# Performance work log

Hardware: AMD Instinct MI355X
Metric: run time of the kernel (lower is better)

## Reference

```python
import jax, jax.numpy as jnp
import numpy as np

NU, NI, ED, H = 30000, 10000, 64, 4
D = ED * H            # fusion_dim = 256
N = NU + NI           # total graph nodes
E = 100000            # edges
B = 8192              # scored (user, wine) pairs
NST, SD = 4, 64       # side tokens / side token dim
NEG = -1e30


def setup_inputs():
    key = jax.random.key(0)
    ks = iter(jax.random.split(key, 64))

    def w(*shape):
        return jax.random.normal(next(ks), shape, jnp.float32) * 0.05

    return {
        "user": jax.random.randint(next(ks), (B,), 0, NU),
        "wine": jax.random.randint(next(ks), (B,), 0, NI),
        "edge_index": jax.random.randint(next(ks), (2, E), 0, N),
        "keep_edge": jax.random.uniform(next(ks), (E,)) > 0.2,   # edge_dropout keep mask
        "node_mask": jax.random.uniform(next(ks), (N,)) < 0.2,   # mask-autoencoding mask
        "user_emb": w(NU, ED),
        "wine_emb": w(NI, ED),
        "up_w": w(ED, D), "up_b": w(D),
        "wp_w": w(ED, D), "wp_b": w(D),
        "sf_proj_w": w(SD, D), "sf_proj_b": w(D),
        "sf_q_w": w(D, D), "sf_q_b": w(D),
        "sf_k_w": w(D, D), "sf_k_b": w(D),
        "sf_v_w": w(D, D), "sf_v_b": w(D),
        "sf_o_w": w(D, D), "sf_o_b": w(D),
        "sf_fc_w": w(2 * D, D), "sf_fc_b": w(D),
        "g_w": w(D, D), "g_b": w(D),
        "t_q_w": w(D, H * D), "t_q_b": w(H * D),
        "t_k_w": w(D, H * D), "t_k_b": w(H * D),
        "t_v_w": w(D, H * D), "t_v_b": w(H * D),
        "t_skip_w": w(D, D), "t_skip_b": w(D),
        "fc_w": w(2 * D, 1), "fc_b": w(1),
        "ae_w": w(D, D), "ae_b": w(D),
        "ep_w": w(2 * D, 1), "ep_b": w(1),
        "wine_side_features": jax.random.normal(next(ks), (NI, NST, SD), jnp.float32),
    }


def _forward(user, wine, edge_index, keep_edge, node_mask,
             user_emb, wine_emb, up_w, up_b, wp_w, wp_b,
             sf_proj_w, sf_proj_b, sf_q_w, sf_q_b, sf_k_w, sf_k_b,
             sf_v_w, sf_v_b, sf_o_w, sf_o_b, sf_fc_w, sf_fc_b,
             g_w, g_b, t_q_w, t_q_b, t_k_w, t_k_b, t_v_w, t_v_b,
             t_skip_w, t_skip_b, fc_w, fc_b, ae_w, ae_b, ep_w, ep_b,
             wine_side_features):
    u_proj = user_emb @ up_w + up_b                       # [NU, D]
    w_proj = wine_emb @ wp_w + wp_b                       # [NI, D]

    # WineSideFusion: single-head attention of wine embedding over side tokens
    side = wine_side_features @ sf_proj_w + sf_proj_b     # [NI, T, D]
    q = w_proj @ sf_q_w + sf_q_b                          # [NI, D]
    k = side @ sf_k_w + sf_k_b                            # [NI, T, D]
    v = side @ sf_v_w + sf_v_b
    attn = jax.nn.softmax(jnp.einsum('nd,ntd->nt', q, k) / jnp.sqrt(jnp.float32(D)), axis=-1)
    ao = jnp.einsum('nt,ntd->nd', attn, v) @ sf_o_w + sf_o_b
    fused = jnp.concatenate([w_proj, ao], axis=1) @ sf_fc_w + sf_fc_b

    x = jnp.concatenate([u_proj, fused], axis=0)          # [N, D]
    src, dst = edge_index[0], edge_index[1]
    ew = keep_edge.astype(x.dtype)                        # edge dropout as 0/1 weights

    # GCNConv (add self loops, symmetric norm)
    deg = jax.ops.segment_sum(ew, dst, num_segments=N) + 1.0
    dinv = jax.lax.rsqrt(deg)
    norm = dinv[src] * dinv[dst] * ew                     # [E]
    xw = x @ g_w                                          # [N, D]
    agg = jax.ops.segment_sum(xw[src] * norm[:, None], dst, num_segments=N)
    x = agg + xw * (dinv * dinv)[:, None] + g_b

    # TransformerConv(heads=H, concat=False): mean over heads + skip
    qh = (x @ t_q_w + t_q_b).reshape(N, H, D)
    kh = (x @ t_k_w + t_k_b).reshape(N, H, D)
    vh = (x @ t_v_w + t_v_b).reshape(N, H, D)
    logits = jnp.einsum('ehd,ehd->eh', qh[dst], kh[src]) / jnp.sqrt(jnp.float32(D))
    logits = jnp.where(keep_edge[:, None], logits, NEG)
    m = jax.ops.segment_max(logits, dst, num_segments=N)  # [N, H]
    m = jnp.where(m < NEG / 2, 0.0, m)                    # guard empty segments
    e = jnp.exp(logits - m[dst]) * ew[:, None]            # [E, H]
    den = jax.ops.segment_sum(e, dst, num_segments=N)     # [N, H]
    num = jax.ops.segment_sum(e[:, :, None] * vh[src], dst, num_segments=N)  # [N, H, D]
    attn_out = num / jnp.maximum(den, 1e-16)[:, :, None]
    x = attn_out.mean(axis=1) + x @ t_skip_w + t_skip_b   # [N, D]

    # Masked autoencoding: masked rows are zeroed, then autoencoded -> recon = bias
    maskf = node_mask.astype(x.dtype)
    recon = ae_b                                          # 0 @ ae_w + ae_b
    diff = recon[None, :] - x                             # [N, D]
    recon_loss = jnp.sum(maskf[:, None] * diff * diff) / (jnp.sum(maskf) * D)

    u_out = x[user]                                       # [B, D]
    w_out = x[wine + NU]                                  # [B, D]
    pair = jnp.concatenate([u_out, w_out], axis=1)        # [B, 2D]

    edge_score = jax.nn.sigmoid(pair @ ep_w + ep_b)       # [B, 1]
    edge_pred_loss = jnp.mean((edge_score - 1.0) ** 2)

    score = jax.nn.sigmoid((pair @ fc_w + fc_b).squeeze(-1)) * 4.0 + 1.0  # [B]
    return score, recon_loss, edge_pred_loss


def reference(user, wine, edge_index, keep_edge, node_mask,
              user_emb, wine_emb, up_w, up_b, wp_w, wp_b,
              sf_proj_w, sf_proj_b, sf_q_w, sf_q_b, sf_k_w, sf_k_b,
              sf_v_w, sf_v_b, sf_o_w, sf_o_b, sf_fc_w, sf_fc_b,
              g_w, g_b, t_q_w, t_q_b, t_k_w, t_k_b, t_v_w, t_v_b,
              t_skip_w, t_skip_b, fc_w, fc_b, ae_w, ae_b, ep_w, ep_b,
              wine_side_features):
    return _forward(user, wine, edge_index, keep_edge, node_mask,
                    user_emb, wine_emb, up_w, up_b, wp_w, wp_b,
                    sf_proj_w, sf_proj_b, sf_q_w, sf_q_b, sf_k_w, sf_k_b,
                    sf_v_w, sf_v_b, sf_o_w, sf_o_b, sf_fc_w, sf_fc_b,
                    g_w, g_b, t_q_w, t_q_b, t_k_w, t_k_b, t_v_w, t_v_b,
                    t_skip_w, t_skip_b, fc_w, fc_b, ae_w, ae_b, ep_w, ep_b,
                    wine_side_features)
```

## Files before the change

### kernel.cpp

```cpp
#include <hip/hip_runtime.h>
#include <stdint.h>

typedef unsigned short u16;
typedef unsigned char u8;
typedef __attribute__((ext_vector_type(8))) short bf16x8;
typedef __attribute__((ext_vector_type(4))) float f32x4;

#define NU_C 30000
#define NI_C 10000
#define N_C  40000
#define E_C  100000
#define B_C  8192

static __device__ __forceinline__ float bf2f(u16 u) {
    union { unsigned int i; float f; } c; c.i = ((unsigned int)u) << 16; return c.f;
}
static __device__ __forceinline__ u16 f2bf(float f) {
    union { float f; unsigned int i; } c; c.f = f;
    return (u16)((c.i + 0x7FFFu + ((c.i >> 16) & 1u)) >> 16);
}
static __device__ __forceinline__ float wave_sum(float v) {
#pragma unroll
    for (int off = 32; off > 0; off >>= 1) v += __shfl_xor(v, off);
    return v;
}
static __device__ __forceinline__ float group_sum16(float v) {
#pragma unroll
    for (int off = 8; off > 0; off >>= 1) v += __shfl_xor(v, off);
    return v;
}
static __device__ __forceinline__ float dot16(const bf16x8 a0, const bf16x8 a1,
                                              const bf16x8 b0, const bf16x8 b1) {
    float p = 0.f;
#pragma unroll
    for (int j = 0; j < 8; ++j) p = fmaf(bf2f((u16)a0[j]), bf2f((u16)b0[j]), p);
#pragma unroll
    for (int j = 0; j < 8; ++j) p = fmaf(bf2f((u16)a1[j]), bf2f((u16)b1[j]), p);
    return p;
}

__global__ void zero_kernel(unsigned int* p, int n) {
    int i = blockIdx.x * 256 + threadIdx.x;
    if (i < n) p[i] = 0u;
}
__global__ void fillval_kernel(float* p, int n, float v) {
    int i = blockIdx.x * 256 + threadIdx.x;
    if (i < n) p[i] = v;
}

__global__ void detect_kernel(const unsigned int* a, int n, int* flag) {
    int i = blockIdx.x * 256 + threadIdx.x;
    if (i >= n) return;
    unsigned int v = a[i];
    int f = 0;
    if (v > 1u) f |= 1;
    if (v != 0u && v != 0x3F800000u) f |= 2;
    if (f) atomicOr(flag, f);
}
__global__ void conv_masks_kernel(const void* keep_raw, const void* nm_raw,
                                  u8* km, u8* nm, int E, int N, const int* flag)
{
    int i = blockIdx.x * 256 + threadIdx.x;
    const int f = *flag;
    if (i < E) {
        u8 r;
        if ((f & 1) == 0)      r = ((const int*)keep_raw)[i] != 0;
        else if ((f & 2) == 0) r = ((const float*)keep_raw)[i] != 0.f;
        else                   r = ((const u8*)keep_raw)[i] != 0;
        km[i] = r;
    }
    int j = i - E;
    if (j >= 0 && j < N) {
        u8 r;
        if ((f & 1) == 0)      r = ((const int*)nm_raw)[j] != 0;
        else if ((f & 2) == 0) r = ((const float*)nm_raw)[j] != 0.f;
        else                   r = ((const u8*)nm_raw)[j] != 0;
        nm[j] = r;
    }
}

__global__ void conv3_kernel(const float* __restrict__ a, int na4,
                             const float* __restrict__ b, int nb4,
                             const float* __restrict__ c, int nc4,
                             u16* __restrict__ oa, u16* __restrict__ ob, u16* __restrict__ oc)
{
    int tot = na4 + nb4 + nc4;
    for (int i = blockIdx.x * 256 + threadIdx.x; i < tot; i += gridDim.x * 256) {
        const float* s; u16* o; int j = i;
        if (j < na4) { s = a; o = oa; }
        else if ((j -= na4) < nb4) { s = b; o = ob; }
        else { j -= nb4; s = c; o = oc; }
        float4 v = *(const float4*)&s[(size_t)j * 4];
        ushort4 r;
        r.x = f2bf(v.x); r.y = f2bf(v.y); r.z = f2bf(v.z); r.w = f2bf(v.w);
        *(ushort4*)&o[(size_t)j * 4] = r;
    }
}

#define WT_ELEMS 1359872
__device__ const int wd_prefix[23] = {0,16384,32768,49152,114688,180224,245760,311296,442368,
    507904,573440,638976,704512,770048,835584,901120,966656,1032192,1097728,1163264,1228800,
    1294336,1359872};
__device__ const u8  wd_src[22]  = {0,1,2,3,4,5,6,7,8,9,10,11,12,10,11,12,10,11,12,10,11,12};
__device__ const short wd_ldw[22]= {256,256,256,256,256,256,256,256,256,256,
    1024,1024,1024,1024,1024,1024,1024,1024,1024,1024,1024,1024};
__device__ const short wd_coff[22]={0,0,0,0,0,0,0,0,0,0, 0,0,0, 256,256,256, 512,512,512, 768,768,768};
__device__ const short wd_kmask[22]={63,63,63,255,255,255,255,511,255,255,
    255,255,255,255,255,255,255,255,255,255,255,255};
__device__ const u8  wd_ksh[22] = {6,6,6,8,8,8,8,9,8,8, 8,8,8,8,8,8,8,8,8,8,8,8};

__global__ __launch_bounds__(256)
void wtrans_kernel(const float* w0, const float* w1, const float* w2, const float* w3,
                   const float* w4, const float* w5, const float* w6, const float* w7,
                   const float* w8, const float* w9, const float* w10, const float* w11,
                   const float* w12, u16* __restrict__ WT)
{
    int idx = blockIdx.x * 256 + threadIdx.x;
    if (idx >= WT_ELEMS) return;
    int d = 0;
    while (wd_prefix[d + 1] <= idx) ++d;
    const int local = idx - wd_prefix[d];
    const int k = local & wd_kmask[d];
    const int n = local >> wd_ksh[d];
    const float* s;
    switch (wd_src[d]) {
        case 0: s = w0; break; case 1: s = w1; break; case 2: s = w2; break;
        case 3: s = w3; break; case 4: s = w4; break; case 5: s = w5; break;
        case 6: s = w6; break; case 7: s = w7; break; case 8: s = w8; break;
        case 9: s = w9; break; case 10: s = w10; break; case 11: s = w11; break;
        default: s = w12; break;
    }
    WT[idx] = f2bf(s[(size_t)k * wd_ldw[d] + wd_coff[d] + n]);
}

__global__ void prep_bias_kernel(const float* sfk_b, const float* sfv_b,
                                 const float* tq_b, const float* tk_b, const float* tv_b,
                                 float* kvb, float* qkvb)
{
    int i = blockIdx.x * 256 + threadIdx.x;
    if (i < 512) kvb[i] = i < 256 ? sfk_b[i] : sfv_b[i - 256];
    if (i < 3072) {
        int h = i / 768, j = i - h * 768;
        qkvb[i] = j < 256 ? tq_b[h * 256 + j]
                : (j < 512 ? tk_b[h * 256 + j - 256] : tv_b[h * 256 + j - 512]);
    }
}

template <typename OT>
__global__ __launch_bounds__(512)
void mgemm_kernel(const u16* __restrict__ A, int lda,
                  const u16* __restrict__ WT,
                  const float* __restrict__ bias,
                  OT* __restrict__ C, int ldc,
                  int M, int N, int K)
{
    __shared__ __align__(16) u16 As[256][72];
    __shared__ __align__(16) u16 Bs[128][72];
    const int t = threadIdx.x;
    const int wid = t >> 6, lane = t & 63;
    const int wr = wid >> 1, wc = wid & 1;
    const int lr = lane & 15, lg = lane >> 4;
    const int gx = gridDim.x;
    const int nwg = gx * gridDim.y;
    const int orig = blockIdx.y * gx + blockIdx.x;
    const int q8 = nwg >> 3, r8 = nwg & 7;
    const int xcd = orig & 7, oidx = orig >> 3;
    const int swzb = (xcd < r8 ? xcd * (q8 + 1) : r8 * (q8 + 1) + (xcd - r8) * q8) + oidx;
    const int row0 = (swzb / gx) * 256, col0 = (swzb % gx) * 128;
    const int sra = t >> 1, sha = (t & 1) * 32;
    const int srb = t >> 2, shb = (t & 3) * 16;
    const bool avalid = (row0 + sra) < M;
    const u16* aptr = &A[(size_t)min(row0 + sra, M - 1) * lda];
    const u16* bptr = &WT[(size_t)(col0 + srb) * K];
    const bf16x8 z = {0, 0, 0, 0, 0, 0, 0, 0};
    f32x4 acc[4][4] = {};
    bf16x8 ra[4], rb[2];

    auto gload = [&](int k0) {
#pragma unroll
        for (int j = 0; j < 4; ++j)
            ra[j] = avalid ? *(const bf16x8*)&aptr[k0 + sha + j * 8] : z;
#pragma unroll
        for (int j = 0; j < 2; ++j)
            rb[j] = *(const bf16x8*)&bptr[k0 + shb + j * 8];
    };
    auto swrite = [&]() {
#pragma unroll
        for (int j = 0; j < 4; ++j)
            *(bf16x8*)&As[sra][sha + j * 8] = ra[j];
#pragma unroll
        for (int j = 0; j < 2; ++j)
            *(bf16x8*)&Bs[srb][shb + j * 8] = rb[j];
    };
    auto compute = [&]() {
#pragma unroll
        for (int kk = 0; kk < 2; ++kk) {
            bf16x8 af[4], bfr[4];
#pragma unroll
            for (int m = 0; m < 4; ++m)
                af[m] = *(const bf16x8*)&As[wr * 64 + m * 16 + lr][kk * 32 + lg * 8];
#pragma unroll
            for (int n = 0; n < 4; ++n)
                bfr[n] = *(const bf16x8*)&Bs[wc * 64 + n * 16 + lr][kk * 32 + lg * 8];
#pragma unroll
            for (int m = 0; m < 4; ++m)
#pragma unroll
                for (int n = 0; n < 4; ++n)
                    acc[m][n] = __builtin_amdgcn_mfma_f32_16x16x32_bf16(af[m], bfr[n], acc[m][n], 0, 0, 0);
        }
    };

    gload(0);
    swrite();
    __syncthreads();
    for (int k0 = 64; k0 < K; k0 += 64) {
        gload(k0);
        compute();
        __syncthreads();
        swrite();
        __syncthreads();
    }
    compute();

#pragma unroll
    for (int m = 0; m < 4; ++m) {
#pragma unroll
        for (int r = 0; r < 4; ++r) {
            int row = row0 + wr * 64 + m * 16 + lg * 4 + r;
            if (row >= M) continue;
#pragma unroll
            for (int n = 0; n < 4; ++n) {
                int col = col0 + wc * 64 + n * 16 + lr;
                float v = acc[m][n][r];
                if (bias) v += bias[col];
                if constexpr (sizeof(OT) == 4) C[(size_t)row * ldc + col] = v;
                else C[(size_t)row * ldc + col] = f2bf(v);
            }
        }
    }
}

__global__ __launch_bounds__(256)
void side_attn_kernel(const u16* __restrict__ q, const u16* __restrict__ kv,
                      u16* __restrict__ ao, int NI)
{
    const int wid = threadIdx.x >> 6, lane = threadIdx.x & 63;
    const int n = blockIdx.x * 4 + wid;
    if (n >= NI) return;
    const ushort4 qu = *(const ushort4*)&q[(size_t)n * 256 + lane * 4];
    const float q0 = bf2f(qu.x), q1 = bf2f(qu.y), q2 = bf2f(qu.z), q3 = bf2f(qu.w);
    float logit[4];
#pragma unroll
    for (int tk = 0; tk < 4; ++tk) {
        const ushort4 ku = *(const ushort4*)&kv[((size_t)n * 4 + tk) * 512 + lane * 4];
        float p = q0 * bf2f(ku.x) + q1 * bf2f(ku.y) + q2 * bf2f(ku.z) + q3 * bf2f(ku.w);
        logit[tk] = wave_sum(p) * (1.f / 16.f);
    }
    float mx = fmaxf(fmaxf(logit[0], logit[1]), fmaxf(logit[2], logit[3]));
    float e[4], den = 0.f;
#pragma unroll
    for (int tk = 0; tk < 4; ++tk) { e[tk] = __expf(logit[tk] - mx); den += e[tk]; }
    const float inv = 1.f / den;
    float o0 = 0.f, o1 = 0.f, o2 = 0.f, o3 = 0.f;
#pragma unroll
    for (int tk = 0; tk < 4; ++tk) {
        const ushort4 vu = *(const ushort4*)&kv[((size_t)n * 4 + tk) * 512 + 256 + lane * 4];
        const float w = e[tk] * inv;
        o0 = fmaf(w, bf2f(vu.x), o0); o1 = fmaf(w, bf2f(vu.y), o1);
        o2 = fmaf(w, bf2f(vu.z), o2); o3 = fmaf(w, bf2f(vu.w), o3);
    }
    ushort4 o;
    o.x = f2bf(o0); o.y = f2bf(o1); o.z = f2bf(o2); o.w = f2bf(o3);
    *(ushort4*)&ao[(size_t)n * 256 + lane * 4] = o;
}

__global__ void count_kernel(const int* __restrict__ dst, const u8* __restrict__ keep,
                             int* __restrict__ cnt, float* __restrict__ degw, int E)
{
    int e = blockIdx.x * 256 + threadIdx.x;
    if (e >= E) return;
    int d = dst[e];
    atomicAdd(&cnt[d], 1);
    if (keep[e]) atomicAdd(&degw[d], 1.f);
}

__global__ void dinv_kernel(const float* __restrict__ degw, float* __restrict__ dinv, int N)
{
    int n = blockIdx.x * 256 + threadIdx.x;
    if (n < N) dinv[n] = rsqrtf(degw[n] + 1.f);
}

__global__ __launch_bounds__(1024)
void scan_kernel(const int* __restrict__ cnt, int* __restrict__ rs, int n)
{
    __shared__ int wsum[17];
    __shared__ int s_run;
    const int t = threadIdx.x, lane = t & 63, wid = t >> 6;
    if (t == 0) s_run = 0;
    __syncthreads();
    for (int base = 0; base < n; base += 1024) {
        int i = base + t;
        int v = (i < n) ? cnt[i] : 0;
        int x = v;
#pragma unroll
        for (int off = 1; off < 64; off <<= 1) {
            int y = __shfl_up(x, off);
            if (lane >= off) x += y;
        }
        if (lane == 63) wsum[wid] = x;
        __syncthreads();
        if (t == 0) {
            int a = 0;
            for (int j = 0; j < 16; ++j) { int tmp = wsum[j]; wsum[j] = a; a += tmp; }
            wsum[16] = a;
        }
        __syncthreads();
        if (i < n) rs[i] = s_run + wsum[wid] + x - v;
        __syncthreads();
        if (t == 0) s_run += wsum[16];
        __syncthreads();
    }
    if (t == 0) rs[n] = s_run;
}

__global__ void fill_kernel(const int* __restrict__ dst, const int* __restrict__ rs,
                            int* __restrict__ cursor, int* __restrict__ eid, int E)
{
    int e = blockIdx.x * 256 + threadIdx.x;
    if (e >= E) return;
    int d = dst[e];
    int p = atomicAdd(&cursor[d], 1);
    eid[rs[d] + p] = e;
}

__global__ void sort_kernel(const int* __restrict__ rs, int* __restrict__ eid, int N)
{
    int n = blockIdx.x * 256 + threadIdx.x;
    if (n >= N) return;
    const int b = rs[n], len = rs[n + 1] - b;
    for (int i = 1; i < len; ++i) {
        int key = eid[b + i];
        int j = i - 1;
        while (j >= 0 && eid[b + j] > key) { eid[b + j + 1] = eid[b + j]; --j; }
        eid[b + j + 1] = key;
    }
}

__global__ void edge_prep_kernel(const int* __restrict__ eid, const int* __restrict__ src,
                                 const int* __restrict__ dst, const u8* __restrict__ keep,
                                 const float* __restrict__ dinv,
                                 int* __restrict__ ssrc, float* __restrict__ wnorm, int E)
{
    int i = blockIdx.x * 256 + threadIdx.x;
    if (i >= E) return;
    const int e = eid[i];
    const int s = src[e];
    const u8 k = keep[e];
    ssrc[i] = s * 2 + (int)k;
    wnorm[i] = k ? dinv[s] * dinv[dst[e]] : 0.f;
}

__global__ __launch_bounds__(256)
void gcn_kernel(const u16* __restrict__ xw, const int* __restrict__ ssrc,
                const float* __restrict__ wnorm, const int* __restrict__ rs,
                const float* __restrict__ dinv, const float* __restrict__ gb,
                u16* __restrict__ xout, int N)
{
    const int wid = threadIdx.x >> 6, lane = threadIdx.x & 63;
    const int n = blockIdx.x * 4 + wid;
    if (n >= N) return;
    const float di = dinv[n];
    const float dii = di * di;
    const ushort4 own = *(const ushort4*)&xw[(size_t)n * 256 + lane * 4];
    float a0 = bf2f(own.x) * dii, a1 = bf2f(own.y) * dii;
    float a2 = bf2f(own.z) * dii, a3 = bf2f(own.w) * dii;
    const int e0 = rs[n], e1 = rs[n + 1];
    int i = e0;
    for (; i + 1 < e1; i += 2) {
        const float wa = wnorm[i], wb = wnorm[i + 1];
        const int sa = ssrc[i] >> 1, sb = ssrc[i + 1] >> 1;
        const ushort4 ra = *(const ushort4*)&xw[(size_t)sa * 256 + lane * 4];
        const ushort4 rb = *(const ushort4*)&xw[(size_t)sb * 256 + lane * 4];
        a0 = fmaf(bf2f(rb.x), wb, fmaf(bf2f(ra.x), wa, a0));
        a1 = fmaf(bf2f(rb.y), wb, fmaf(bf2f(ra.y), wa, a1));
        a2 = fmaf(bf2f(rb.z), wb, fmaf(bf2f(ra.z), wa, a2));
        a3 = fmaf(bf2f(rb.w), wb, fmaf(bf2f(ra.w), wa, a3));
    }
    if (i < e1) {
        const float wa = wnorm[i];
        const int sa = ssrc[i] >> 1;
        const ushort4 r = *(const ushort4*)&xw[(size_t)sa * 256 + lane * 4];
        a0 = fmaf(bf2f(r.x), wa, a0); a1 = fmaf(bf2f(r.y), wa, a1);
        a2 = fmaf(bf2f(r.z), wa, a2); a3 = fmaf(bf2f(r.w), wa, a3);
    }
    const float4 g = *(const float4*)&gb[lane * 4];
    ushort4 o;
    o.x = f2bf(a0 + g.x); o.y = f2bf(a1 + g.y);
    o.z = f2bf(a2 + g.z); o.w = f2bf(a3 + g.w);
    *(ushort4*)&xout[(size_t)n * 256 + lane * 4] = o;
}

__global__ __launch_bounds__(256)
void tconv_head_kernel(const u16* __restrict__ qkv, const int* __restrict__ ssrc,
                       const int* __restrict__ rs, float* __restrict__ xacc, int N)
{
    const int wid = threadIdx.x >> 6, lane = threadIdx.x & 63;
    const int g = lane >> 4, s = lane & 15;
    const int n = blockIdx.x * 16 + wid * 4 + g;
    if (n >= N) return;
    const bf16x8 qa = *(const bf16x8*)&qkv[(size_t)n * 768 + s * 16];
    const bf16x8 qb = *(const bf16x8*)&qkv[(size_t)n * 768 + s * 16 + 8];
    const int e0 = rs[n], e1 = rs[n + 1];
    float m = -1e30f, den = 0.f;
    float ac[16] = {};
    int i = e0;
    for (; i + 1 < e1; i += 2) {
        const int va = ssrc[i], vb = ssrc[i + 1];
        const size_t sa = (size_t)(va >> 1) * 768, sb = (size_t)(vb >> 1) * 768;
        const float ewa = (float)(va & 1), ewb = (float)(vb & 1);
        const bf16x8 ka0 = *(const bf16x8*)&qkv[sa + 256 + s * 16];
        const bf16x8 ka1 = *(const bf16x8*)&qkv[sa + 256 + s * 16 + 8];
        const bf16x8 kb0 = *(const bf16x8*)&qkv[sb + 256 + s * 16];
        const bf16x8 kb1 = *(const bf16x8*)&qkv[sb + 256 + s * 16 + 8];
        const bf16x8 xa0 = *(const bf16x8*)&qkv[sa + 512 + s * 16];
        const bf16x8 xa1 = *(const bf16x8*)&qkv[sa + 512 + s * 16 + 8];
        const bf16x8 xb0 = *(const bf16x8*)&qkv[sb + 512 + s * 16];
        const bf16x8 xb1 = *(const bf16x8*)&qkv[sb + 512 + s * 16 + 8];
        float pa = group_sum16(dot16(qa, qb, ka0, ka1)) * (1.f / 16.f);
        float pb = group_sum16(dot16(qa, qb, kb0, kb1)) * (1.f / 16.f);
        {
            const float mn = fmaxf(m, pa);
            const float sc = __expf(m - mn);
            const float w = __expf(pa - mn) * ewa;
            den = den * sc + w;
#pragma unroll
            for (int j = 0; j < 8; ++j) ac[j] = fmaf(w, bf2f((u16)xa0[j]), ac[j] * sc);
#pragma unroll
            for (int j = 0; j < 8; ++j) ac[8 + j] = fmaf(w, bf2f((u16)xa1[j]), ac[8 + j] * sc);
            m = mn;
        }
        {
            const float mn = fmaxf(m, pb);
            const float sc = __expf(m - mn);
            const float w = __expf(pb - mn) * ewb;
            den = den * sc + w;
#pragma unroll
            for (int j = 0; j < 8; ++j) ac[j] = fmaf(w, bf2f((u16)xb0[j]), ac[j] * sc);
#pragma unroll
            for (int j = 0; j < 8; ++j) ac[8 + j] = fmaf(w, bf2f((u16)xb1[j]), ac[8 + j] * sc);
            m = mn;
        }
    }
    if (i < e1) {
        const int va = ssrc[i];
        const size_t sa = (size_t)(va >> 1) * 768;
        const float ewa = (float)(va & 1);
        const bf16x8 ka0 = *(const bf16x8*)&qkv[sa + 256 + s * 16];
        const bf16x8 ka1 = *(const bf16x8*)&qkv[sa + 256 + s * 16 + 8];
        const bf16x8 xa0 = *(const bf16x8*)&qkv[sa + 512 + s * 16];
        const bf16x8 xa1 = *(const bf16x8*)&qkv[sa + 512 + s * 16 + 8];
        float pa = group_sum16(dot16(qa, qb, ka0, ka1)) * (1.f / 16.f);
        const float mn = fmaxf(m, pa);
        const float sc = __expf(m - mn);
        const float w = __expf(pa - mn) * ewa;
        den = den * sc + w;
#pragma unroll
        for (int j = 0; j < 8; ++j) ac[j] = fmaf(w, bf2f((u16)xa0[j]), ac[j] * sc);
#pragma unroll
        for (int j = 0; j < 8; ++j) ac[8 + j] = fmaf(w, bf2f((u16)xa1[j]), ac[8 + j] * sc);
    }
    const float inv = 0.25f / fmaxf(den, 1e-16f);
    float4* p4 = (float4*)&xacc[(size_t)n * 256 + s * 16];
#pragma unroll
    for (int q = 0; q < 4; ++q) {
        float4 cur = p4[q];
        cur.x += ac[q * 4 + 0] * inv; cur.y += ac[q * 4 + 1] * inv;
        cur.z += ac[q * 4 + 2] * inv; cur.w += ac[q * 4 + 3] * inv;
        p4[q] = cur;
    }
}

__global__ __launch_bounds__(256)
void recon_kernel(const float* __restrict__ x, const u8* __restrict__ mask,
                  const float* __restrict__ aeb,
                  float* __restrict__ rblkS, float* __restrict__ rblkC, int N)
{
    const int total = N * 256;
    float s = 0.f, c = 0.f;
    for (int idx = blockIdx.x * 256 + threadIdx.x; idx < total; idx += gridDim.x * 256) {
        const int n = idx >> 8, d = idx & 255;
        if (mask[n]) {
            const float diff = aeb[d] - x[idx];
            s = fmaf(diff, diff, s);
            if (d == 0) c += 1.f;
        }
    }
    s = wave_sum(s); c = wave_sum(c);
    __shared__ float ss[4], cc[4];
    const int lane = threadIdx.x & 63, wid = threadIdx.x >> 6;
    if (lane == 0) { ss[wid] = s; cc[wid] = c; }
    __syncthreads();
    if (threadIdx.x == 0) {
        rblkS[blockIdx.x] = ss[0] + ss[1] + ss[2] + ss[3];
        rblkC[blockIdx.x] = cc[0] + cc[1] + cc[2] + cc[3];
    }
}

__global__ __launch_bounds__(256)
void score_kernel(const float* __restrict__ x, const int* __restrict__ user,
                  const int* __restrict__ wine,
                  const float* __restrict__ epw, const float* __restrict__ epb,
                  const float* __restrict__ fcw, const float* __restrict__ fcb,
                  float* __restrict__ out, float* __restrict__ sblk, int B)
{
    __shared__ float sep[4];
    const int wid = threadIdx.x >> 6, lane = threadIdx.x & 63;
    const int b = blockIdx.x * 4 + wid;
    if (b < B) {
        const size_t u = (size_t)user[b];
        const size_t w = (size_t)wine[b] + NU_C;
        const float4 xu = *(const float4*)&x[u * 256 + lane * 4];
        const float4 xw = *(const float4*)&x[w * 256 + lane * 4];
        const float4 e1 = *(const float4*)&epw[lane * 4];
        const float4 e2 = *(const float4*)&epw[256 + lane * 4];
        const float4 f1 = *(const float4*)&fcw[lane * 4];
        const float4 f2 = *(const float4*)&fcw[256 + lane * 4];
        float pep = xu.x * e1.x + xu.y * e1.y + xu.z * e1.z + xu.w * e1.w
                  + xw.x * e2.x + xw.y * e2.y + xw.z * e2.z + xw.w * e2.w;
        float pfc = xu.x * f1.x + xu.y * f1.y + xu.z * f1.z + xu.w * f1.w
                  + xw.x * f2.x + xw.y * f2.y + xw.z * f2.z + xw.w * f2.w;
        pep = wave_sum(pep); pfc = wave_sum(pfc);
        if (lane == 0) {
            const float es = 1.f / (1.f + __expf(-(pep + epb[0])));
            sep[wid] = (es - 1.f) * (es - 1.f);
            out[b] = 1.f / (1.f + __expf(-(pfc + fcb[0]))) * 4.f + 1.f;
        }
    } else if (lane == 0) {
        sep[wid] = 0.f;
    }
    __syncthreads();
    if (threadIdx.x == 0) sblk[blockIdx.x] = sep[0] + sep[1] + sep[2] + sep[3];
}

__global__ __launch_bounds__(1024)
void final_reduce_kernel(const float* __restrict__ rblkS, const float* __restrict__ rblkC,
                         const float* __restrict__ sblk, float* __restrict__ out, int B)
{
    const int t = threadIdx.x, lane = t & 63, wid = t >> 6;
    float s = rblkS[t] + rblkS[t + 1024];
    float c = rblkC[t] + rblkC[t + 1024];
    float p = sblk[t] + sblk[t + 1024];
    s = wave_sum(s); c = wave_sum(c); p = wave_sum(p);
    __shared__ float ss[16], cc[16], pp[16];
    if (lane == 0) { ss[wid] = s; cc[wid] = c; pp[wid] = p; }
    __syncthreads();
    if (t == 0) {
        float S = 0.f, C = 0.f, P = 0.f;
        for (int i = 0; i < 16; ++i) { S += ss[i]; C += cc[i]; P += pp[i]; }
        out[B] = S / (C * 256.f);
        out[B + 1] = P / (float)B;
    }
}

extern "C" void kernel_launch(void* const* d_in, const int* in_sizes, int n_in,
                              void* d_out, int out_size, void* d_ws, size_t ws_size,
                              hipStream_t stream)
{
    const int* user = (const int*)d_in[0];
    const int* wine = (const int*)d_in[1];
    const int* e_src = (const int*)d_in[2];
    const int* e_dst = e_src + E_C;
    const void* keep_raw  = d_in[3];
    const void* nmask_raw = d_in[4];
    const float* user_emb = (const float*)d_in[5];
    const float* wine_emb = (const float*)d_in[6];
    const float* up_w = (const float*)d_in[7];
    const float* up_b = (const float*)d_in[8];
    const float* wp_w = (const float*)d_in[9];
    const float* wp_b = (const float*)d_in[10];
    const float* sf_proj_w = (const float*)d_in[11];
    const float* sf_proj_b = (const float*)d_in[12];
    const float* sf_q_w = (const float*)d_in[13];
    const float* sf_q_b = (const float*)d_in[14];
    const float* sf_k_w = (const float*)d_in[15];
    const float* sf_k_b = (const float*)d_in[16];
    const float* sf_v_w = (const float*)d_in[17];
    const float* sf_v_b = (const float*)d_in[18];
    const float* sf_o_w = (const float*)d_in[19];
    const float* sf_o_b = (const float*)d_in[20];
    const float* sf_fc_w = (const float*)d_in[21];
    const float* sf_fc_b = (const float*)d_in[22];
    const float* g_w = (const float*)d_in[23];
    const float* g_b = (const float*)d_in[24];
    const float* t_q_w = (const float*)d_in[25];
    const float* t_q_b = (const float*)d_in[26];
    const float* t_k_w = (const float*)d_in[27];
    const float* t_k_b = (const float*)d_in[28];
    const float* t_v_w = (const float*)d_in[29];
    const float* t_v_b = (const float*)d_in[30];
    const float* t_skip_w = (const float*)d_in[31];
    const float* t_skip_b = (const float*)d_in[32];
    const float* fc_w = (const float*)d_in[33];
    const float* fc_b = (const float*)d_in[34];
    const float* ae_b = (const float*)d_in[36];
    const float* ep_w = (const float*)d_in[37];
    const float* ep_b = (const float*)d_in[38];
    const float* wsf = (const float*)d_in[39];
    float* out = (float*)d_out;
    char* ws = (char*)d_ws;

    size_t off = 0;
    auto take = [&](size_t b) { size_t r = off; off += (b + 255) & ~(size_t)255; return r; };
    const size_t o_xb     = take((size_t)N_C * 256 * 2);
    const size_t o_cnt    = take((size_t)N_C * 4);
    const size_t o_degw   = take((size_t)N_C * 4);
    const size_t o_cursor = take((size_t)N_C * 4);
    const size_t o_scal   = take(256);
    const size_t o_rowst  = take((size_t)(N_C + 1) * 4);
    const size_t o_dinv   = take((size_t)N_C * 4);
    const size_t o_eid    = take((size_t)E_C * 4);
    const size_t o_ssrc   = take((size_t)E_C * 4);
    const size_t o_wnorm  = take((size_t)E_C * 4);
    const size_t o_kmask  = take((size_t)E_C);
    const size_t o_nmask  = take((size_t)N_C);
    const size_t o_rblkS  = take(2048 * 4);
    const size_t o_rblkC  = take(2048 * 4);
    const size_t o_sblk   = take(2048 * 4);
    const size_t o_wt     = take((size_t)WT_ELEMS * 2);
    const size_t o_bias   = take(3584 * 4);
    const size_t ARENA    = 102400000;
    const size_t o_arena  = take(ARENA);
    const size_t NEED = off;

    if (ws_size < NEED) {
        fillval_kernel<<<dim3((out_size + 255) / 256), 256, 0, stream>>>(
            out, out_size, (float)((double)ws_size / (1024.0 * 1024.0)));
        return;
    }

    u16*   xb     = (u16*)  (ws + o_xb);
    int*   cnt    = (int*)  (ws + o_cnt);
    float* degw   = (float*)(ws + o_degw);
    int*   cursor = (int*)  (ws + o_cursor);
    int*   flag   = (int*)  (ws + o_scal);
    int*   rowst  = (int*)  (ws + o_rowst);
    float* dinvb  = (float*)(ws + o_dinv);
    int*   eid    = (int*)  (ws + o_eid);
    int*   ssrc   = (int*)  (ws + o_ssrc);
    float* wnorm  = (float*)(ws + o_wnorm);
    u8*    kmask  = (u8*)   (ws + o_kmask);
    u8*    nmaskb = (u8*)   (ws + o_nmask);
    float* rblkS  = (float*)(ws + o_rblkS);
    float* rblkC  = (float*)(ws + o_rblkC);
    float* sblk   = (float*)(ws + o_sblk);
    u16*   WT     = (u16*)  (ws + o_wt);
    float* kvb    = (float*)(ws + o_bias);
    float* qkvb   = kvb + 512;

    u16* wt_up   = WT + 0;
    u16* wt_wp   = WT + 16384;
    u16* wt_proj = WT + 32768;
    u16* wt_sfq  = WT + 49152;
    u16* wt_sfkv = WT + 114688;
    u16* wt_sfo  = WT + 245760;
    u16* wt_sffc = WT + 311296;
    u16* wt_g    = WT + 442368;
    u16* wt_skip = WT + 507904;
    u16* wt_qkv  = WT + 573440;

    u16* ue16  = (u16*)(ws + o_arena);
    u16* we16  = (u16*)(ws + o_arena + 3840000);
    u16* wsf16 = (u16*)(ws + o_arena + 5120000);
    u16* cat   = (u16*)(ws + o_arena + 10240000);
    u16* side  = (u16*)(ws + o_arena + 20480000);
    u16* qbuf  = (u16*)(ws + o_arena + 40960000);
    u16* kvbuf = (u16*)(ws + o_arena + 46080000);
    u16* aobuf = (u16*)(ws + o_arena + 87040000);
    u16* xw    = (u16*)(ws + o_arena);
    u16* qkvh  = (u16*)(ws + o_arena);
    float* xacc = (float*)(ws + o_arena + 61440000);

    const int zero_words = (3 * N_C * 4 + 256) / 4;
    zero_kernel<<<dim3((zero_words + 255) / 256), 256, 0, stream>>>((unsigned int*)cnt, zero_words);

    detect_kernel<<<dim3((E_C / 4 + 255) / 256), 256, 0, stream>>>((const unsigned int*)keep_raw, E_C / 4, flag);
    conv_masks_kernel<<<dim3((E_C + N_C + 255) / 256), 256, 0, stream>>>(keep_raw, nmask_raw, kmask, nmaskb, E_C, N_C, flag);

    conv3_kernel<<<dim3(2048), 256, 0, stream>>>(user_emb, NU_C * 16, wine_emb, NI_C * 16,
                                                 wsf, N_C * 16, ue16, we16, wsf16);
    wtrans_kernel<<<dim3(WT_ELEMS / 256), 256, 0, stream>>>(up_w, wp_w, sf_proj_w, sf_q_w,
        sf_k_w, sf_v_w, sf_o_w, sf_fc_w, g_w, t_skip_w, t_q_w, t_k_w, t_v_w, WT);
    prep_bias_kernel<<<dim3(12), 256, 0, stream>>>(sf_k_b, sf_v_b, t_q_b, t_k_b, t_v_b, kvb, qkvb);

    mgemm_kernel<u16><<<dim3(2, 118), 512, 0, stream>>>(ue16, 64, wt_up, up_b, xb, 256, NU_C, 256, 64);
    mgemm_kernel<u16><<<dim3(2, 40), 512, 0, stream>>>(we16, 64, wt_wp, wp_b, cat, 512, NI_C, 256, 64);
    mgemm_kernel<u16><<<dim3(2, 157), 512, 0, stream>>>(wsf16, 64, wt_proj, sf_proj_b, side, 256, N_C, 256, 64);
    mgemm_kernel<u16><<<dim3(2, 40), 512, 0, stream>>>(cat, 512, wt_sfq, sf_q_b, qbuf, 256, NI_C, 256, 256);
    mgemm_kernel<u16><<<dim3(4, 157), 512, 0, stream>>>(side, 256, wt_sfkv, kvb, kvbuf, 512, N_C, 512, 256);
    side_attn_kernel<<<dim3(2500), 256, 0, stream>>>(qbuf, kvbuf, aobuf, NI_C);
    mgemm_kernel<u16><<<dim3(2, 40), 512, 0, stream>>>(aobuf, 256, wt_sfo, sf_o_b, cat + 256, 512, NI_C, 256, 256);
    mgemm_kernel<u16><<<dim3(2, 40), 512, 0, stream>>>(cat, 512, wt_sffc, sf_fc_b, xb + (size_t)NU_C * 256, 256, NI_C, 256, 512);

    count_kernel<<<dim3((E_C + 255) / 256), 256, 0, stream>>>(e_dst, kmask, cnt, degw, E_C);
    dinv_kernel<<<dim3((N_C + 255) / 256), 256, 0, stream>>>(degw, dinvb, N_C);
    scan_kernel<<<dim3(1), 1024, 0, stream>>>(cnt, rowst, N_C);
    fill_kernel<<<dim3((E_C + 255) / 256), 256, 0, stream>>>(e_dst, rowst, cursor, eid, E_C);
    sort_kernel<<<dim3((N_C + 255) / 256), 256, 0, stream>>>(rowst, eid, N_C);
    edge_prep_kernel<<<dim3((E_C + 255) / 256), 256, 0, stream>>>(eid, e_src, e_dst, kmask, dinvb, ssrc, wnorm, E_C);

    mgemm_kernel<u16><<<dim3(2, 157), 512, 0, stream>>>(xb, 256, wt_g, nullptr, xw, 256, N_C, 256, 256);
    gcn_kernel<<<dim3(N_C / 4), 256, 0, stream>>>(xw, ssrc, wnorm, rowst, dinvb, g_b, xb, N_C);

    mgemm_kernel<float><<<dim3(2, 157), 512, 0, stream>>>(xb, 256, wt_skip, t_skip_b, xacc, 256, N_C, 256, 256);
    for (int h = 0; h < 4; ++h) {
        mgemm_kernel<u16><<<dim3(6, 157), 512, 0, stream>>>(xb, 256, wt_qkv + h * 196608,
                                                            qkvb + h * 768, qkvh, 768, N_C, 768, 256);
        tconv_head_kernel<<<dim3(N_C / 16), 256, 0, stream>>>(qkvh, ssrc, rowst, xacc, N_C);
    }

    recon_kernel<<<dim3(2048), 256, 0, stream>>>(xacc, nmaskb, ae_b, rblkS, rblkC, N_C);
    score_kernel<<<dim3(2048), 256, 0, stream>>>(xacc, user, wine, ep_w, ep_b, fc_w, fc_b, out, sblk, B_C);
    final_reduce_kernel<<<dim3(1), 1024, 0, stream>>>(rblkS, rblkC, sblk, out, B_C);
}
```

Baseline: 610.6 us.

## Batch all four transformer-head QKV GEMMs and fuse per-head attention into one kernel

```diff
diff --git a/kernel.cpp b/kernel.cpp
--- a/kernel.cpp
+++ b/kernel.cpp
@@ -398,6 +398,93 @@
     o.x = f2bf(a0 + g.x); o.y = f2bf(a1 + g.y);
     o.z = f2bf(a2 + g.z); o.w = f2bf(a3 + g.w);
     *(ushort4*)&xout[(size_t)n * 256 + lane * 4] = o;
+}
+
+__global__ __launch_bounds__(256)
+void tconv_all_kernel(const u16* __restrict__ qkv, const int* __restrict__ ssrc,
+                      const int* __restrict__ rs, float* __restrict__ xacc, int N)
+{
+    const int wid = threadIdx.x >> 6, lane = threadIdx.x & 63;
+    const int g = lane >> 4, s = lane & 15;
+    const int n = blockIdx.x * 16 + wid * 4 + g;
+    if (n >= N) return;
+    const int e0 = rs[n], e1 = rs[n + 1];
+    float fin[16] = {};
+    for (int h = 0; h < 4; ++h) {
+        const size_t qb0 = (size_t)n * 3072 + h * 768;
+        const bf16x8 qa = *(const bf16x8*)&qkv[qb0 + s * 16];
+        const bf16x8 qb = *(const bf16x8*)&qkv[qb0 + s * 16 + 8];
+        float m = -1e30f, den = 0.f;
+        float ac[16] = {};
+        int i = e0;
+        for (; i + 1 < e1; i += 2) {
+            const int va = ssrc[i], vb = ssrc[i + 1];
+            const size_t sa = (size_t)(va >> 1) * 3072 + h * 768;
+            const size_t sb = (size_t)(vb >> 1) * 3072 + h * 768;
+            const float ewa = (float)(va & 1), ewb = (float)(vb & 1);
+            const bf16x8 ka0 = *(const bf16x8*)&qkv[sa + 256 + s * 16];
+            const bf16x8 ka1 = *(const bf16x8*)&qkv[sa + 256 + s * 16 + 8];
+            const bf16x8 kb0 = *(const bf16x8*)&qkv[sb + 256 + s * 16];
+            const bf16x8 kb1 = *(const bf16x8*)&qkv[sb + 256 + s * 16 + 8];
+            const bf16x8 xa0 = *(const bf16x8*)&qkv[sa + 512 + s * 16];
+            const bf16x8 xa1 = *(const bf16x8*)&qkv[sa + 512 + s * 16 + 8];
+            const bf16x8 xb0 = *(const bf16x8*)&qkv[sb + 512 + s * 16];
+            const bf16x8 xb1 = *(const bf16x8*)&qkv[sb + 512 + s * 16 + 8];
+            float pa = group_sum16(dot16(qa, qb, ka0, ka1)) * (1.f / 16.f);
+            float pb = group_sum16(dot16(qa, qb, kb0, kb1)) * (1.f / 16.f);
+            {
+                const float mn = fmaxf(m, pa);
+                const float sc = __expf(m - mn);
+                const float w = __expf(pa - mn) * ewa;
+                den = den * sc + w;
+#pragma unroll
+                for (int j = 0; j < 8; ++j) ac[j] = fmaf(w, bf2f((u16)xa0[j]), ac[j] * sc);
+#pragma unroll
+                for (int j = 0; j < 8; ++j) ac[8 + j] = fmaf(w, bf2f((u16)xa1[j]), ac[8 + j] * sc);
+                m = mn;
+            }
+            {
+                const float mn = fmaxf(m, pb);
+                const float sc = __expf(m - mn);
+                const float w = __expf(pb - mn) * ewb;
+                den = den * sc + w;
+#pragma unroll
+                for (int j = 0; j < 8; ++j) ac[j] = fmaf(w, bf2f((u16)xb0[j]), ac[j] * sc);
+#pragma unroll
+                for (int j = 0; j < 8; ++j) ac[8 + j] = fmaf(w, bf2f((u16)xb1[j]), ac[8 + j] * sc);
+                m = mn;
+            }
+        }
+        if (i < e1) {
+            const int va = ssrc[i];
+            const size_t sa = (size_t)(va >> 1) * 3072 + h * 768;
+            const float ewa = (float)(va & 1);
+            const bf16x8 ka0 = *(const bf16x8*)&qkv[sa + 256 + s * 16];
+            const bf16x8 ka1 = *(const bf16x8*)&qkv[sa + 256 + s * 16 + 8];
+            const bf16x8 xa0 = *(const bf16x8*)&qkv[sa + 512 + s * 16];
+            const bf16x8 xa1 = *(const bf16x8*)&qkv[sa + 512 + s * 16 + 8];
+            float pa = group_sum16(dot16(qa, qb, ka0, ka1)) * (1.f / 16.f);
+            const float mn = fmaxf(m, pa);
+            const float sc = __expf(m - mn);
+            const float w = __expf(pa - mn) * ewa;
+            den = den * sc + w;
+#pragma unroll
+            for (int j = 0; j < 8; ++j) ac[j] = fmaf(w, bf2f((u16)xa0[j]), ac[j] * sc);
+#pragma unroll
+            for (int j = 0; j < 8; ++j) ac[8 + j] = fmaf(w, bf2f((u16)xa1[j]), ac[8 + j] * sc);
+        }
+        const float inv = 0.25f / fmaxf(den, 1e-16f);
+#pragma unroll
+        for (int j = 0; j < 16; ++j) fin[j] += ac[j] * inv;
+    }
+    float4* p4 = (float4*)&xacc[(size_t)n * 256 + s * 16];
+#pragma unroll
+    for (int q = 0; q < 4; ++q) {
+        float4 cur = p4[q];
+        cur.x += fin[q * 4 + 0]; cur.y += fin[q * 4 + 1];
+        cur.z += fin[q * 4 + 2]; cur.w += fin[q * 4 + 3];
+        p4[q] = cur;
+    }
 }
 
 __global__ __launch_bounds__(256)
@@ -628,9 +715,12 @@
     const size_t o_sblk   = take(2048 * 4);
     const size_t o_wt     = take((size_t)WT_ELEMS * 2);
     const size_t o_bias   = take(3584 * 4);
-    const size_t ARENA    = 102400000;
-    const size_t o_arena  = take(ARENA);
+    const size_t ARENA_SMALL = 102400000;
+    const size_t ARENA_BIG   = 286720000;
+    const size_t o_arena  = take(ARENA_SMALL);
     const size_t NEED = off;
+    const size_t NEED_BIG = NEED - ARENA_SMALL + ARENA_BIG;
+    const bool big = ws_size >= NEED_BIG;
 
     if (ws_size < NEED) {
         fillval_kernel<<<dim3((out_size + 255) / 256), 256, 0, stream>>>(
@@ -678,7 +768,10 @@
     u16* aobuf = (u16*)(ws + o_arena + 87040000);
     u16* xw    = (u16*)(ws + o_arena);
     u16* qkvh  = (u16*)(ws + o_arena);
-    float* xacc = (float*)(ws + o_arena + 61440000);
+    float* xacc_s = (float*)(ws + o_arena + 61440000);
+    u16* qkv4  = (u16*)(ws + o_arena);
+    float* xacc_b = (float*)(ws + o_arena + 245760000);
+    float* xacc = big ? xacc_b : xacc_s;
 
     const int zero_words = (3 * N_C * 4 + 256) / 4;
     zero_kernel<<<dim3((zero_words + 255) / 256), 256, 0, stream>>>((unsigned int*)cnt, zero_words);
@@ -712,10 +805,15 @@
     gcn_kernel<<<dim3(N_C / 4), 256, 0, stream>>>(xw, ssrc, wnorm, rowst, dinvb, g_b, xb, N_C);
 
     mgemm_kernel<float><<<dim3(2, 157), 512, 0, stream>>>(xb, 256, wt_skip, t_skip_b, xacc, 256, N_C, 256, 256);
-    for (int h = 0; h < 4; ++h) {
-        mgemm_kernel<u16><<<dim3(6, 157), 512, 0, stream>>>(xb, 256, wt_qkv + h * 196608,
-                                                            qkvb + h * 768, qkvh, 768, N_C, 768, 256);
-        tconv_head_kernel<<<dim3(N_C / 16), 256, 0, stream>>>(qkvh, ssrc, rowst, xacc, N_C);
+    if (big) {
+        mgemm_kernel<u16><<<dim3(24, 157), 512, 0, stream>>>(xb, 256, wt_qkv, qkvb, qkv4, 3072, N_C, 3072, 256);
+        tconv_all_kernel<<<dim3(N_C / 16), 256, 0, stream>>>(qkv4, ssrc, rowst, xacc, N_C);
+    } else {
+        for (int h = 0; h < 4; ++h) {
+            mgemm_kernel<u16><<<dim3(6, 157), 512, 0, stream>>>(xb, 256, wt_qkv + h * 196608,
+                                                                qkvb + h * 768, qkvh, 768, N_C, 768, 256);
+            tconv_head_kernel<<<dim3(N_C / 16), 256, 0, stream>>>(qkvh, ssrc, rowst, xacc, N_C);
+        }
     }
 
     recon_kernel<<<dim3(2048), 256, 0, stream>>>(xacc, nmaskb, ae_b, rblkS, rblkC, N_C);
```

Measured after the change: 610.0 us, median of 3. No clear change (-0.1%).
